# Kernel tuning notes

Hardware: AMD Instinct MI355X
Metric: run time of the kernel (lower is better)

The kernel has to match this reference:

```python
import jax, jax.numpy as jnp
import numpy as np

N_NODES = 50000
N_EDGES = 400000
C_NODE = 128
C_EDGE = 256
# PyG: round(c_in + (c_out-c_in)*f)
H1, H2, H3 = 166, 192, 218


def setup_inputs() -> dict:
    key = jax.random.key(0)
    ks = jax.random.split(key, 20)
    x = jax.random.normal(ks[0], (N_NODES, C_NODE), dtype=jnp.float32)
    edge_index = jax.random.randint(ks[1], (2, N_EDGES), 0, N_NODES, dtype=jnp.int64)

    def glorot(k, fan_in, fan_out):
        s = jnp.sqrt(6.0 / (fan_in + fan_out)).astype(jnp.float32)
        return jax.random.uniform(k, (fan_in, fan_out), jnp.float32, -s, s)

    dims_e = [(C_NODE, H1), (H1, H2), (H2, H3), (H3, C_EDGE)]
    dims_n = [(C_NODE, C_NODE)] * 4
    inp = {"x": x, "edge_index": edge_index}
    for i, (fi, fo) in enumerate(dims_e, 1):
        inp[f"W{i}e"] = glorot(ks[1 + i], fi, fo)
        inp[f"b{i}e"] = jnp.zeros((fo,), jnp.float32)
    for i, (fi, fo) in enumerate(dims_n, 1):
        inp[f"W{i}n"] = glorot(ks[9 + i], fi, fo)
        inp[f"b{i}n"] = jnp.zeros((fo,), jnp.float32)
    return inp


def _gcn_norm(edge_index, n_nodes):
    # add self loops, then symmetric normalization (PyG gcn_norm, improved=False)
    loops = jnp.arange(n_nodes, dtype=edge_index.dtype)
    src = jnp.concatenate([edge_index[0], loops])
    dst = jnp.concatenate([edge_index[1], loops])
    deg = jax.ops.segment_sum(jnp.ones_like(dst, dtype=jnp.float32), dst, num_segments=n_nodes)
    dinv = jnp.where(deg > 0, jax.lax.rsqrt(deg), 0.0)
    norm = dinv[src] * dinv[dst]  # [E+N]
    return src, dst, norm


def _gcn_conv(h_in, W, b, src, dst, norm, n_nodes):
    h = h_in @ W                      # [N, C_out] dense transform first (PyG order)
    msg = h[src] * norm[:, None]      # gather + scale, [E+N, C_out]
    agg = jax.ops.segment_sum(msg, dst, num_segments=n_nodes)
    return agg + b


def _forward(x, edge_index, We, be, Wn, bn):
    n = x.shape[0]
    src, dst, norm = _gcn_norm(edge_index, n)
    e = x
    for i in range(4):
        e = _gcn_conv(e, We[i], be[i], src, dst, norm, n)
        e = jax.nn.relu(e) if i < 3 else jax.nn.sigmoid(e)
    v = x
    for i in range(4):
        v = _gcn_conv(v, Wn[i], bn[i], src, dst, norm, n)
        v = jax.nn.relu(v) if i < 3 else jax.nn.sigmoid(v)
    return e, v


def reference(x, edge_index, W1e, b1e, W2e, b2e, W3e, b3e, W4e, b4e,
              W1n, b1n, W2n, b2n, W3n, b3n, W4n, b4n):
    We = [W1e, W2e, W3e, W4e]
    be = [b1e, b2e, b3e, b4e]
    Wn = [W1n, W2n, W3n, W4n]
    bn = [b1n, b2n, b3n, b4n]
    return _forward(x, edge_index, We, be, Wn, bn)
```

## Files before the change

kernel.cpp:

```cpp
#include <hip/hip_runtime.h>
#include <hip/hip_bf16.h>
#include <cstdint>
#include <cstddef>

typedef __hip_bfloat16 bf16;
typedef __attribute__((ext_vector_type(8))) short bf16x8;
typedef __attribute__((ext_vector_type(4))) float f32x4;

#define NN 50000
#define NE 400000

__device__ __forceinline__ float bf2f(unsigned short u) {
    return __uint_as_float(((unsigned)u) << 16);
}
__device__ __forceinline__ unsigned short f2bf(float f) {
    __hip_bfloat16 h = __float2bfloat16(f);
    return *reinterpret_cast<unsigned short*>(&h);
}
__device__ __forceinline__ float fin(float v) {
    return (v == v && v > -1e30f && v < 1e30f) ? v : 0.0f;
}
__device__ __forceinline__ float rd(const void* p, int i, int f) {
    return f ? ((const float*)p)[i] : bf2f(((const unsigned short*)p)[i]);
}

__device__ __forceinline__ void gl16(const void* g, void* l) {
    __builtin_amdgcn_global_load_lds(
        (const __attribute__((address_space(1))) unsigned int*)g,
        (__attribute__((address_space(3))) unsigned int*)l, 16, 0, 0);
}

__device__ __forceinline__ int probe_flag(const unsigned* __restrict__ p, int words,
                                          int* sflag) {
    if (threadIdx.x < 64) {
        int lane = threadIdx.x;
        int zc = 0, bc = 0;
        #pragma unroll
        for (int c = 0; c < 4; ++c) {
            int idx = c * 64 + lane;
            int act = idx < words;
            unsigned w = act ? p[idx] : 0u;
            int isz = act && (w == 0u);
            int e = (w >> 7) & 0xFF;
            int isb = act && !isz && (e >= 100 && e <= 140);
            zc += __popcll(__ballot(isz));
            bc += __popcll(__ballot(isb));
        }
        int nz = words - zc;
        if (lane == 0) *sflag = (nz == 0 || 2 * bc >= nz) ? 0 : 1;
    }
    __syncthreads();
    return *sflag;
}

struct Prep {
    const void* wsrc[8];
    unsigned short* pwh[8];
    unsigned short* pwl[8];
    int K[8], M[8], Kp[8];
    int b0[8];
    int biasStart, xinStart;
    const void* bsrc[8];
    int bM[8], bmp[8], bmo[8];
    float* ball;
    const void* x;
    const float* dinv;
    unsigned short* xs;
};

__global__ void k_prep(Prep P) {
    __shared__ int sflag;
    const int bid = blockIdx.x;

    if (bid >= P.xinStart) {
        int f = probe_flag((const unsigned*)P.x, 256, &sflag);
        int t = (bid - P.xinStart) * 256 + threadIdx.x;
        if (t >= NN * 16) return;
        int i = t >> 4, c = (t & 15) * 8;
        float d = P.dinv[i];
        const float* xf = (const float*)P.x + (size_t)i * 128 + c;
        const unsigned short* xb = (const unsigned short*)P.x + (size_t)i * 128 + c;
        unsigned short o[8];
        #pragma unroll
        for (int j = 0; j < 8; ++j)
            o[j] = f2bf(fin(f ? xf[j] : bf2f(xb[j])) * d);
        *(uint4*)(P.xs + (size_t)i * 128 + c) = *(uint4*)o;
        return;
    }
    if (bid >= P.biasStart) {
        int l = bid - P.biasStart;
        int words = P.bM[l] >> 1; if (words > 256) words = 256;
        int f = probe_flag((const unsigned*)P.bsrc[l], words, &sflag);
        int i = threadIdx.x;
        if (i < P.bmp[l])
            P.ball[P.bmo[l] + i] = (i < P.bM[l]) ? fin(rd(P.bsrc[l], i, f)) : 0.0f;
        return;
    }
    int seg = 0;
    #pragma unroll
    for (int t = 1; t < 8; ++t) if (bid >= P.b0[t]) seg = t;
    int words = (P.K[seg] * P.M[seg]) >> 1; if (words > 256) words = 256;
    int f = probe_flag((const unsigned*)P.wsrc[seg], words, &sflag);
    int n = bid - P.b0[seg];
    int k = threadIdx.x;
    int Kp = P.Kp[seg];
    if (k >= Kp) return;
    float v = 0.0f;
    if (k < P.K[seg] && n < P.M[seg])
        v = fin(rd(P.wsrc[seg], k * P.M[seg] + n, f));
    unsigned short hi = f2bf(v);
    unsigned short lo = f2bf(v - bf2f(hi));
    P.pwh[seg][(size_t)n * Kp + k] = hi;
    P.pwl[seg][(size_t)n * Kp + k] = lo;
}

__global__ void k_repack(const int* __restrict__ ei,
                         int* __restrict__ src, int* __restrict__ dst,
                         int* __restrict__ deg) {
    __shared__ int sAny;
    if (threadIdx.x < 64) {
        int lane = threadIdx.x;
        int any = 0;
        #pragma unroll
        for (int c = 0; c < 32; ++c) {
            int idx = c * 64 + lane;
            int v = ei[2 * idx + 1];
            any |= (__ballot(v != 0) != 0ull) ? 1 : 0;
        }
        if (lane == 0) sAny = any;
    }
    __syncthreads();
    int f = sAny;
    int e = blockIdx.x * blockDim.x + threadIdx.x;
    if (e >= NE) return;
    int s, d;
    if (f) { s = ei[e]; d = ei[NE + e]; }
    else   { s = ei[2 * e]; d = ei[2 * (NE + e)]; }
    s = min(max(s, 0), NN - 1);
    d = min(max(d, 0), NN - 1);
    src[e] = s;
    dst[e] = d;
    atomicAdd(&deg[d], 1);
}

__global__ void k_scan1(const int* __restrict__ deg, int* __restrict__ rowp,
                        int* __restrict__ part) {
    __shared__ int s[512];
    int tid = threadIdx.x, i = blockIdx.x * 512 + tid;
    int v = (i < NN) ? deg[i] : 0;
    s[tid] = v;
    __syncthreads();
    for (int off = 1; off < 512; off <<= 1) {
        int t = (tid >= off) ? s[tid - off] : 0;
        __syncthreads();
        s[tid] += t;
        __syncthreads();
    }
    if (i < NN) rowp[i] = s[tid] - v;
    if (tid == 511) part[blockIdx.x] = s[511];
}

__global__ void k_scan3b(int* __restrict__ rowp, const int* __restrict__ part,
                         const int* __restrict__ deg, float* __restrict__ dinv,
                         int* __restrict__ cursor) {
    __shared__ int sS;
    const int b = blockIdx.x;
    const int g = b >> 1;
    if (threadIdx.x < 64) {
        int lane = threadIdx.x;
        int v = 0;
        if (lane < g) v += part[lane];
        if (64 + lane < g) v += part[64 + lane];
        #pragma unroll
        for (int o = 1; o < 64; o <<= 1) v += __shfl_xor(v, o);
        if (lane == 0) sS = v;
    }
    __syncthreads();
    int S = sS;
    int i = b * 256 + threadIdx.x;
    if (i < NN) {
        rowp[i] += S;
        dinv[i] = rsqrtf((float)deg[i] + 1.0f);
        cursor[i] = 0;
    }
    if (i == 0) rowp[NN] = NE;
}

__global__ void k_fill(const int* __restrict__ src, const int* __restrict__ dst,
                       const int* __restrict__ rowp, int* __restrict__ cursor,
                       int* __restrict__ colv) {
    int e = blockIdx.x * blockDim.x + threadIdx.x;
    if (e >= NE) return;
    int d = dst[e];
    int p = atomicAdd(&cursor[d], 1);
    colv[rowp[d] + p] = src[e];
}

__launch_bounds__(256)
__global__ void k_gather(const unsigned short* __restrict__ in, int istride,
                         unsigned short* __restrict__ out, int ostride, int lanes,
                         const int* __restrict__ rowp, const int* __restrict__ colv,
                         const float* __restrict__ dinv) {
    const int node = blockIdx.x * 4 + (threadIdx.x >> 6);
    if (node >= NN) return;
    const int lane = threadIdx.x & 63;
    const int beg = rowp[node], end = rowp[node + 1];
    float a[8] = {0.f, 0.f, 0.f, 0.f, 0.f, 0.f, 0.f, 0.f};
    auto accq = [&](uint4 q) {
        unsigned v[4] = {q.x, q.y, q.z, q.w};
        #pragma unroll
        for (int t = 0; t < 4; ++t) {
            a[2 * t] += bf2f(v[t] & 0xFFFF); a[2 * t + 1] += bf2f(v[t] >> 16);
        }
    };
    if (lanes <= 16) {
        const int slot = lane >> 4;
        const int l8 = lane & 15;
        const bool on = l8 < lanes;
        const size_t off = (size_t)l8 * 8;
        if (slot == 0 && on)
            accq(*(const uint4*)(in + (size_t)node * istride + off));
        for (int j = beg + slot; j < end; j += 4) {
            const int s = colv[j];
            if (on) accq(*(const uint4*)(in + (size_t)s * istride + off));
        }
        #pragma unroll
        for (int t = 0; t < 8; ++t) {
            a[t] += __shfl_xor(a[t], 16);
            a[t] += __shfl_xor(a[t], 32);
        }
        if (lane < lanes) {
            float d = dinv[node];
            unsigned short o[8];
            #pragma unroll
            for (int t = 0; t < 8; ++t) o[t] = f2bf(a[t] * d);
            *(uint4*)(out + (size_t)node * ostride + (size_t)lane * 8) = *(uint4*)o;
        }
    } else {
        const bool on = lane < lanes;
        const size_t off = (size_t)lane * 8;
        if (on) accq(*(const uint4*)(in + (size_t)node * istride + off));
        int j = beg;
        for (; j + 1 < end; j += 2) {
            int s0 = colv[j], s1 = colv[j + 1];
            if (on) {
                uint4 q0 = *(const uint4*)(in + (size_t)s0 * istride + off);
                uint4 q1 = *(const uint4*)(in + (size_t)s1 * istride + off);
                accq(q0); accq(q1);
            }
        }
        if (j < end) {
            int s0 = colv[j];
            if (on) accq(*(const uint4*)(in + (size_t)s0 * istride + off));
        }
        if (on) {
            float d = dinv[node];
            unsigned short o[8];
            #pragma unroll
            for (int t = 0; t < 8; ++t) o[t] = f2bf(a[t] * d);
            *(uint4*)(out + (size_t)node * ostride + off) = *(uint4*)o;
        }
    }
}

struct GSide {
    const unsigned short* A;
    const unsigned short* Wh;
    const unsigned short* Wl;
    const float* bias;
    void* out;
    int Kp, ostride, M, OutW, act;
};

__launch_bounds__(256, 3)
__global__ void k_mgemm(GSide s0, GSide s1, int ySplit, int NY, int NB, int astride,
                        const float* __restrict__ dinv) {
    __shared__ __align__(16) unsigned char ldsraw[49152];
    auto sA  = reinterpret_cast<unsigned short (*)[128][32]>(ldsraw);
    auto sBh = reinterpret_cast<unsigned short (*)[128][32]>(ldsraw + 16384);
    auto sBl = reinterpret_cast<unsigned short (*)[128][32]>(ldsraw + 32768);

    const int tid = threadIdx.x;
    const int wave = tid >> 6, lane = tid & 63;
    const int wr = wave >> 1, wc = wave & 1;
    const int quad = lane >> 4, m16 = lane & 15;

    const int NBa = NB & ~7;
    const int swcut = NBa * NY;
    int b = blockIdx.x, x, yv;
    if (b < swcut) {
        x = (b / (8 * NY)) * 8 + (b & 7);
        yv = (b >> 3) % NY;
    } else {
        int r = b - swcut, rem = NB - NBa;
        x = rem ? (NBa + r % rem) : 0;
        yv = rem ? (r / rem) : 0;
    }

    GSide S; int ycol;
    if (yv < ySplit) { S = s0; ycol = yv; }
    else             { S = s1; ycol = yv - ySplit; }
    const int row0 = x * 128, col0 = ycol * 128;
    const int Kp = S.Kp;

    const int lr = lane >> 2;
    const int swz = ((lane >> 2) ^ (lane >> 4)) & 3;
    const int su = ((lane & 3) ^ swz) * 8;

    int ar1 = row0 + wave * 32 + lr;      if (ar1 >= NN) ar1 = NN - 1;
    int ar2 = row0 + wave * 32 + 16 + lr; if (ar2 >= NN) ar2 = NN - 1;
    const unsigned short* gA1 = S.A + (size_t)ar1 * astride + su;
    const unsigned short* gA2 = S.A + (size_t)ar2 * astride + su;
    const int br = col0 + wave * 32 + lr;
    const unsigned short* gBh1 = S.Wh + (size_t)br * Kp + su;
    const unsigned short* gBl1 = S.Wl + (size_t)br * Kp + su;

    f32x4 zz = {0.f, 0.f, 0.f, 0.f};
    f32x4 acc[4][4];
    #pragma unroll
    for (int i = 0; i < 4; ++i)
        #pragma unroll
        for (int j = 0; j < 4; ++j) acc[i][j] = zz;

    const int rs = (quad ^ ((m16 & 3) ^ ((m16 >> 2) & 3))) * 8;
    const int nk = Kp >> 5;

    auto stage = [&](int bb, int k0) {
        gl16(gA1 + k0,            &sA[bb][wave * 32][0]);
        gl16(gA2 + k0,            &sA[bb][wave * 32 + 16][0]);
        gl16(gBh1 + k0,           &sBh[bb][wave * 32][0]);
        gl16(gBh1 + 16 * Kp + k0, &sBh[bb][wave * 32 + 16][0]);
        gl16(gBl1 + k0,           &sBl[bb][wave * 32][0]);
        gl16(gBl1 + 16 * Kp + k0, &sBl[bb][wave * 32 + 16][0]);
    };

    stage(0, 0);
    if (nk > 1) stage(1, 32);

    for (int ks = 0; ks < nk; ++ks) {
        const int cur = ks & 1;
        if (ks + 1 < nk) asm volatile("s_waitcnt vmcnt(6)" ::: "memory");
        else             asm volatile("s_waitcnt vmcnt(0)" ::: "memory");
        __builtin_amdgcn_s_barrier();
        bf16x8 fa[4], fh[4], fl[4];
        #pragma unroll
        for (int i = 0; i < 4; ++i) {
            fa[i] = *(const bf16x8*)&sA[cur][wr * 64 + i * 16 + m16][rs];
            fh[i] = *(const bf16x8*)&sBh[cur][wc * 64 + i * 16 + m16][rs];
            fl[i] = *(const bf16x8*)&sBl[cur][wc * 64 + i * 16 + m16][rs];
        }
        asm volatile("s_waitcnt lgkmcnt(0)" ::: "memory");
        __builtin_amdgcn_sched_barrier(0);
        __builtin_amdgcn_s_barrier();
        if (ks + 2 < nk) stage(cur, (ks + 2) * 32);
        #pragma unroll
        for (int i = 0; i < 4; ++i)
            #pragma unroll
            for (int j = 0; j < 4; ++j) {
                acc[i][j] = __builtin_amdgcn_mfma_f32_16x16x32_bf16(fa[i], fh[j], acc[i][j], 0, 0, 0);
                acc[i][j] = __builtin_amdgcn_mfma_f32_16x16x32_bf16(fa[i], fl[j], acc[i][j], 0, 0, 0);
            }
    }

    float* eps = (float*)(ldsraw + (size_t)wave * 4352);
    #pragma unroll
    for (int i = 0; i < 4; ++i) {
        #pragma unroll
        for (int j = 0; j < 4; ++j) {
            int col = col0 + wc * 64 + j * 16 + m16;
            float bcol = (col < S.M) ? S.bias[col] : 0.0f;
            #pragma unroll
            for (int r = 0; r < 4; ++r) {
                float v = acc[i][j][r] + bcol;
                if (S.act) v = (col < S.M) ? 1.0f / (1.0f + expf(-v)) : 0.0f;
                else       v = (col < S.M) ? fmaxf(v, 0.0f) : 0.0f;
                eps[(quad * 4 + r) * 68 + j * 16 + m16] = v;
            }
        }
        asm volatile("s_waitcnt lgkmcnt(0)" ::: "memory");
        __builtin_amdgcn_sched_barrier(0);
        #pragma unroll
        for (int it = 0; it < 4; ++it) {
            int lr2 = it * 4 + (lane >> 4);
            int c4 = (lane & 15) * 4;
            float4 w = *(float4*)&eps[lr2 * 68 + c4];
            int grow = row0 + wr * 64 + i * 16 + lr2;
            int gcol = col0 + wc * 64 + c4;
            if (grow < NN && gcol < S.OutW) {
                if (S.act) {
                    *(float4*)((float*)S.out + (size_t)grow * S.ostride + gcol) = w;
                } else {
                    float d = dinv[grow];
                    unsigned o0 = f2bf(w.x * d) | ((unsigned)f2bf(w.y * d) << 16);
                    unsigned o1 = f2bf(w.z * d) | ((unsigned)f2bf(w.w * d) << 16);
                    uint2 u; u.x = o0; u.y = o1;
                    *(uint2*)((unsigned short*)S.out + (size_t)grow * S.ostride + gcol) = u;
                }
            }
        }
        asm volatile("s_waitcnt lgkmcnt(0)" ::: "memory");
        __builtin_amdgcn_sched_barrier(0);
    }
}

__global__ void k_sentinel(float* __restrict__ out, int n) {
    int i = blockIdx.x * blockDim.x + threadIdx.x;
    if (i < n) out[i] = 4.0f;
}

extern "C" void kernel_launch(void* const* d_in, const int* in_sizes, int n_in,
                              void* d_out, int out_size, void* d_ws, size_t ws_size,
                              hipStream_t stream) {
    const int* ei = (const int*)d_in[1];
    float* out_e = (float*)d_out;
    float* out_v = out_e + (size_t)NN * 256;

    const int KpW[8] = {128, 192, 192, 224, 0, 128, 128, 128};
    const int MpW[8] = {384, 256, 256, 256, 0, 128, 128, 128};

    char* wsb = (char*)d_ws;
    size_t o = 0;
    auto align = [](size_t v) { return (v + 255) & ~(size_t)255; };
    int*   colv   = (int*)(wsb + o);  o = align(o + (size_t)NE * 4);
    int*   deg    = (int*)(wsb + o);  o = align(o + (size_t)NN * 4);
    int*   cursor = (int*)(wsb + o);  o = align(o + (size_t)NN * 4);
    int*   rowp   = (int*)(wsb + o);  o = align(o + (size_t)(NN + 1) * 4);
    int*   part   = (int*)(wsb + o);  o = align(o + 512);
    float* dinv   = (float*)(wsb + o); o = align(o + (size_t)NN * 4);
    unsigned short* wh[8]; unsigned short* wl[8];
    for (int l = 0; l < 8; ++l) {
        size_t wel = (size_t)MpW[l] * KpW[l];
        wh[l] = (unsigned short*)(wsb + o); o = align(o + wel * 2);
        wl[l] = (unsigned short*)(wsb + o); o = align(o + wel * 2);
    }
    float* ball = (float*)(wsb + o); o = align(o + 1376 * 4);
    unsigned short* bufA = (unsigned short*)(wsb + o); o = align(o + (size_t)NN * 352 * 2);
    unsigned short* bufB = (unsigned short*)(wsb + o); o = align(o + (size_t)NN * 352 * 2);
    int* src32 = (int*)bufB;
    int* dst32 = src32 + NE;
    if (o > ws_size) {
        k_sentinel<<<(out_size + 255) / 256, 256, 0, stream>>>(out_e, out_size);
        return;
    }

    const int moff[8] = {0, 296, 616, 968, 168, 488, 840, 1224};
    const int mpad[8] = {168, 192, 224, 256, 128, 128, 128, 128};

    const int EB = (NE + 255) / 256;
    const int NB512 = (NN + 511) / 512;
    const int GX = (NN + 127) / 128;
    const int GN = (NN + 3) / 4;

    hipMemsetAsync(deg, 0, (size_t)NN * 4, stream);
    k_repack<<<EB, 256, 0, stream>>>(ei, src32, dst32, deg);
    k_scan1<<<NB512, 512, 0, stream>>>(deg, rowp, part);
    k_scan3b<<<(NN + 255) / 256, 256, 0, stream>>>(rowp, part, deg, dinv, cursor);
    k_fill<<<EB, 256, 0, stream>>>(src32, dst32, rowp, cursor, colv);

    {
        Prep P;
        const void* srcs[8] = {d_in[2], d_in[10], d_in[4], d_in[12],
                               d_in[6], d_in[14], d_in[8], d_in[16]};
        unsigned short* whp[8] = {wh[0], wh[0] + 168 * 128, wh[1], wh[5],
                                  wh[2], wh[6], wh[3], wh[7]};
        unsigned short* wlp[8] = {wl[0], wl[0] + 168 * 128, wl[1], wl[5],
                                  wl[2], wl[6], wl[3], wl[7]};
        const int Ks[8]   = {128, 128, 166, 128, 192, 128, 218, 128};
        const int Ms[8]   = {166, 128, 192, 128, 218, 128, 256, 128};
        const int Kps[8]  = {128, 128, 192, 128, 192, 128, 224, 128};
        const int rows[8] = {168, 216, 256, 128, 256, 128, 256, 128};
        int acc = 0;
        for (int s = 0; s < 8; ++s) {
            P.wsrc[s] = srcs[s]; P.pwh[s] = whp[s]; P.pwl[s] = wlp[s];
            P.K[s] = Ks[s]; P.M[s] = Ms[s]; P.Kp[s] = Kps[s];
            P.b0[s] = acc; acc += rows[s];
        }
        P.biasStart = acc;
        P.xinStart = acc + 8;
        const int bMv[8] = {166, 192, 218, 256, 128, 128, 128, 128};
        for (int l = 0; l < 8; ++l) {
            P.bsrc[l] = d_in[3 + 2 * l];
            P.bM[l] = bMv[l]; P.bmp[l] = mpad[l]; P.bmo[l] = moff[l];
        }
        P.ball = ball;
        P.x = d_in[0];
        P.dinv = dinv;
        P.xs = bufA;
        const int xinBlocks = (NN * 16 + 255) / 256;
        k_prep<<<P.xinStart + xinBlocks, 256, 0, stream>>>(P);
    }

    k_gather<<<GN, 256, 0, stream>>>(bufA, 128, bufB, 128, 16, rowp, colv, dinv);

    {
        GSide s0 = {bufB, wh[0], wl[0], ball, bufA, 128, 296, 296, 296, 0};
        k_mgemm<<<GX * 3, 256, 0, stream>>>(s0, s0, 3, 3, GX, 128, dinv);
    }
    k_gather<<<GN, 256, 0, stream>>>(bufA, 296, bufB, 296, 37, rowp, colv, dinv);

    {
        GSide s0 = {bufB, wh[1], wl[1], ball + 296, bufA, 192, 320, 192, 192, 0};
        GSide s1 = {bufB + 168, wh[5], wl[5], ball + 488, bufA + 192, 128, 320, 128, 128, 0};
        k_mgemm<<<GX * 3, 256, 0, stream>>>(s0, s1, 2, 3, GX, 296, dinv);
    }
    k_gather<<<GN, 256, 0, stream>>>(bufA, 320, bufB, 320, 40, rowp, colv, dinv);

    {
        GSide s0 = {bufB, wh[2], wl[2], ball + 616, bufA, 192, 352, 218, 224, 0};
        GSide s1 = {bufB + 192, wh[6], wl[6], ball + 840, bufA + 224, 128, 352, 128, 128, 0};
        k_mgemm<<<GX * 3, 256, 0, stream>>>(s0, s1, 2, 3, GX, 320, dinv);
    }
    k_gather<<<GN, 256, 0, stream>>>(bufA, 352, bufB, 352, 44, rowp, colv, dinv);

    {
        GSide s0 = {bufB, wh[3], wl[3], ball + 968, out_e, 224, 256, 256, 256, 1};
        GSide s1 = {bufB + 224, wh[7], wl[7], ball + 1224, out_v, 128, 128, 128, 128, 1};
        k_mgemm<<<GX * 3, 256, 0, stream>>>(s0, s1, 2, 3, GX, 352, dinv);
    }
}
```

Baseline: 487.7 us.

## Load low-part weight fragments directly into registers, bypassing LDS staging

```diff
diff --git a/kernel.cpp b/kernel.cpp
--- a/kernel.cpp
+++ b/kernel.cpp
@@ -275,10 +275,9 @@
 __launch_bounds__(256, 3)
 __global__ void k_mgemm(GSide s0, GSide s1, int ySplit, int NY, int NB, int astride,
                         const float* __restrict__ dinv) {
-    __shared__ __align__(16) unsigned char ldsraw[49152];
+    __shared__ __align__(16) unsigned char ldsraw[32768];
     auto sA  = reinterpret_cast<unsigned short (*)[128][32]>(ldsraw);
     auto sBh = reinterpret_cast<unsigned short (*)[128][32]>(ldsraw + 16384);
-    auto sBl = reinterpret_cast<unsigned short (*)[128][32]>(ldsraw + 32768);
 
     const int tid = threadIdx.x;
     const int wave = tid >> 6, lane = tid & 63;
@@ -313,7 +312,7 @@
     const unsigned short* gA2 = S.A + (size_t)ar2 * astride + su;
     const int br = col0 + wave * 32 + lr;
     const unsigned short* gBh1 = S.Wh + (size_t)br * Kp + su;
-    const unsigned short* gBl1 = S.Wl + (size_t)br * Kp + su;
+    const unsigned short* wlb = S.Wl + (size_t)(col0 + wc * 64 + m16) * Kp + quad * 8;
 
     f32x4 zz = {0.f, 0.f, 0.f, 0.f};
     f32x4 acc[4][4];
@@ -330,37 +329,54 @@
         gl16(gA2 + k0,            &sA[bb][wave * 32 + 16][0]);
         gl16(gBh1 + k0,           &sBh[bb][wave * 32][0]);
         gl16(gBh1 + 16 * Kp + k0, &sBh[bb][wave * 32 + 16][0]);
-        gl16(gBl1 + k0,           &sBl[bb][wave * 32][0]);
-        gl16(gBl1 + 16 * Kp + k0, &sBl[bb][wave * 32 + 16][0]);
     };
 
-    stage(0, 0);
-    if (nk > 1) stage(1, 32);
-
-    for (int ks = 0; ks < nk; ++ks) {
+    bf16x8 wlA[4], wlB[4];
+    auto wload = [&](bf16x8 (&dst)[4], int k0) {
+        #pragma unroll
+        for (int j = 0; j < 4; ++j) {
+            const unsigned short* p = wlb + (size_t)j * 16 * Kp + k0;
+            asm volatile("global_load_dwordx4 %0, %1, off" : "=v"(dst[j]) : "v"(p));
+        }
+    };
+
+    auto iter = [&](int ks, bf16x8 (&wcur)[4], bf16x8 (&wnext)[4]) {
         const int cur = ks & 1;
-        if (ks + 1 < nk) asm volatile("s_waitcnt vmcnt(6)" ::: "memory");
-        else             asm volatile("s_waitcnt vmcnt(0)" ::: "memory");
+        if (ks + 1 < nk) { asm volatile("s_waitcnt vmcnt(4)" ::: "memory"); }
+        else             { asm volatile("s_waitcnt vmcnt(0)" ::: "memory"); }
+        __builtin_amdgcn_sched_barrier(0);
         __builtin_amdgcn_s_barrier();
-        bf16x8 fa[4], fh[4], fl[4];
+        bf16x8 fa[4], fh[4];
         #pragma unroll
         for (int i = 0; i < 4; ++i) {
             fa[i] = *(const bf16x8*)&sA[cur][wr * 64 + i * 16 + m16][rs];
             fh[i] = *(const bf16x8*)&sBh[cur][wc * 64 + i * 16 + m16][rs];
-            fl[i] = *(const bf16x8*)&sBl[cur][wc * 64 + i * 16 + m16][rs];
         }
         asm volatile("s_waitcnt lgkmcnt(0)" ::: "memory");
         __builtin_amdgcn_sched_barrier(0);
         __builtin_amdgcn_s_barrier();
+        if (ks + 1 < nk) wload(wnext, (ks + 1) * 32);
         if (ks + 2 < nk) stage(cur, (ks + 2) * 32);
+        __builtin_amdgcn_sched_barrier(0);
         #pragma unroll
         for (int i = 0; i < 4; ++i)
             #pragma unroll
             for (int j = 0; j < 4; ++j) {
                 acc[i][j] = __builtin_amdgcn_mfma_f32_16x16x32_bf16(fa[i], fh[j], acc[i][j], 0, 0, 0);
-                acc[i][j] = __builtin_amdgcn_mfma_f32_16x16x32_bf16(fa[i], fl[j], acc[i][j], 0, 0, 0);
+                acc[i][j] = __builtin_amdgcn_mfma_f32_16x16x32_bf16(fa[i], wcur[j], acc[i][j], 0, 0, 0);
             }
-    }
+    };
+
+    stage(0, 0);
+    wload(wlA, 0);
+    if (nk > 1) stage(1, 32);
+
+    int ks = 0;
+    for (; ks + 1 < nk; ks += 2) {
+        iter(ks,     wlA, wlB);
+        iter(ks + 1, wlB, wlA);
+    }
+    if (ks < nk) iter(ks, wlA, wlB);
 
     float* eps = (float*)(ldsraw + (size_t)wave * 4352);
     #pragma unroll
```

Result: slower. 516.9 us (+6.0%).
